# Optimization experiments

Hardware: AMD Instinct MI355X
Metric: run time of the kernel (lower is better)

Reference implementation:

```python
import jax, jax.numpy as jnp
import numpy as np

B, P, K_NN, HEADS = 4, 2048, 30, 3
N = B * P


def knn_nbr(feat):
    """Per-cloud exact KNN (no self), returns [N, K_NN+1] global neighbor idx, self appended last.
    Matches torch_geometric knn_graph (loop=False) followed by GATConv add_self_loops=True."""
    f = feat.reshape(B, P, -1)
    sq = jnp.sum(f * f, axis=-1)  # [B,P]
    d = sq[:, :, None] + sq[:, None, :] - 2.0 * jnp.einsum('bpc,bqc->bpq', f, f)
    d = d + jnp.eye(P, dtype=f.dtype)[None] * 1e9  # exclude self
    idx = jax.lax.top_k(-d, K_NN)[1]  # [B,P,K_NN] nearest neighbors
    idx = (idx + (jnp.arange(B) * P)[:, None, None]).reshape(N, K_NN)
    return jnp.concatenate([idx, jnp.arange(N)[:, None]], axis=1)  # self-loop last


def gat(xf, nbr, W, a_src, a_dst, bias):
    """PyG GATConv (v1, concat=True, negative_slope=0.2). nbr: [N,K] incoming sources per node."""
    H, F = a_src.shape
    xh = (xf @ W).reshape(N, H, F)
    s = jnp.sum(xh * a_src, axis=-1)  # [N,H] source scores
    t = jnp.sum(xh * a_dst, axis=-1)  # [N,H] target scores
    e = jax.nn.leaky_relu(s[nbr] + t[:, None, :], 0.2)  # [N,K,H]
    alpha = jax.nn.softmax(e, axis=1)  # edge-softmax over incoming edges
    out = jnp.einsum('nkh,nkhf->nhf', alpha, xh[nbr])
    return out.reshape(N, H * F) + bias


def setup_inputs() -> dict:
    key = jax.random.key(0)
    ks = jax.random.split(key, 48)
    w = lambda k, shape: (jax.random.normal(k, shape, jnp.float32) * 0.1)
    H = HEADS
    inp = {
        'x': jax.random.normal(ks[0], (N, 3), jnp.float32),
        'pos': jax.random.normal(ks[1], (N, 3), jnp.float32),
        'batch': (jnp.arange(N) // P).astype(jnp.int32),
        'w1': w(ks[2], (6, 64 * H)), 'as1': w(ks[3], (H, 64)), 'ad1': w(ks[4], (H, 64)), 'b1': w(ks[5], (64 * H,)),
        'ml1w': w(ks[6], (64 * H, 64)), 'ml1b': w(ks[7], (64,)),
        'w2': w(ks[8], (70, 64 * H)), 'as2': w(ks[9], (H, 64)), 'ad2': w(ks[10], (H, 64)), 'b2': w(ks[11], (64 * H,)),
        'ml2w': w(ks[12], (64 * H, 64)), 'ml2b': w(ks[13], (64,)),
        'w3': w(ks[14], (134, 64 * H)), 'as3': w(ks[15], (H, 64)), 'ad3': w(ks[16], (H, 64)), 'b3': w(ks[17], (64 * H,)),
        'ml3w': w(ks[18], (64 * H, 64)), 'ml3b': w(ks[19], (64,)),
        'w4': w(ks[20], (198, 128 * H)), 'as4': w(ks[21], (H, 128)), 'ad4': w(ks[22], (H, 128)), 'b4': w(ks[23], (128 * H,)),
        'ml4w': w(ks[24], (128 * H, 128)), 'ml4b': w(ks[25], (128,)),
        # fe_mlp: 326 -> 1024 -> 1024 (plain last)
        'few1': w(ks[26], (326, 1024)), 'feb1': w(ks[27], (1024,)),
        'few2': w(ks[28], (1024, 1024)), 'feb2': w(ks[29], (1024,)),
        # head mlp: 1350 -> 256 -> 256 -> 128 -> 50
        'mw1': w(ks[30], (1350, 256)), 'mb1': w(ks[31], (256,)),
        'mw2': w(ks[32], (256, 256)), 'mb2': w(ks[33], (256,)),
        'mw3': w(ks[34], (256, 128)), 'mb3': w(ks[35], (128,)),
        'mw4': w(ks[36], (128, 50)), 'mb4': w(ks[37], (50,)),
    }
    return inp


def reference(x, pos, batch,
              w1, as1, ad1, b1, ml1w, ml1b,
              w2, as2, ad2, b2, ml2w, ml2b,
              w3, as3, ad3, b3, ml3w, ml3b,
              w4, as4, ad4, b4, ml4w, ml4b,
              few1, feb1, few2, feb2,
              mw1, mb1, mw2, mb2, mw3, mb3, mw4, mb4):
    x0 = jnp.concatenate([x, pos], axis=-1)  # [N,6]
    nbr = knn_nbr(x0)
    x1 = gat(x0, nbr, w1, as1, ad1, b1) @ ml1w + ml1b  # [N,64]
    nbr = knn_nbr(x1)
    x2 = gat(jnp.concatenate([x0, x1], 1), nbr, w2, as2, ad2, b2) @ ml2w + ml2b
    nbr = knn_nbr(x2)
    x3 = gat(jnp.concatenate([x0, x1, x2], 1), nbr, w3, as3, ad3, b3) @ ml3w + ml3b
    nbr = knn_nbr(x2)  # faithful to source: 4th graph also built from x2
    x4 = gat(jnp.concatenate([x0, x1, x2, x3], 1), nbr, w4, as4, ad4, b4) @ ml4w + ml4b
    link4 = jnp.concatenate([x0, x1, x2, x3, x4], axis=-1)  # [N,326]
    h = jax.nn.relu(link4 @ few1 + feb1) @ few2 + feb2  # [N,1024]
    g = jnp.max(h, axis=0, keepdims=True)  # global feature (dropout=eval identity)
    lg = jnp.concatenate([link4, jnp.broadcast_to(g, (N, h.shape[1]))], axis=1)
    h = jax.nn.relu(lg @ mw1 + mb1)
    h = jax.nn.relu(h @ mw2 + mb2)
    h = jax.nn.relu(h @ mw3 + mb3)
    out = h @ mw4 + mb4
    return jax.nn.log_softmax(out, axis=1)
```

## Files before the change

kernel.cpp:

```cpp
#include <hip/hip_runtime.h>
#include <hip/hip_bf16.h>
#include <hip/amd_detail/amd_hip_vector_types.h>

#define NPTS 8192
#define PP 2048
#define KNN 30
#define KTOT 31
#define HEADS 3
#define LDH 352
#define NSEG 9
#define LDZ 200
#define LDZB3 200
#define LDZB4 392

typedef __attribute__((ext_vector_type(8))) short short8;
typedef __attribute__((ext_vector_type(4))) float floatx4;
typedef __attribute__((ext_vector_type(4))) unsigned int uint4_t;
typedef unsigned short ushort_t;
typedef unsigned int uint_t;

__device__ inline ushort_t f2bs(float v) {
    __hip_bfloat16 b = __float2bfloat16(v);
    return *reinterpret_cast<ushort_t*>(&b);
}
__device__ inline float bs2f(ushort_t u) {
    __hip_bfloat16 b = *reinterpret_cast<__hip_bfloat16*>(&u);
    return __bfloat162float(b);
}
__device__ inline void split2(float v, ushort_t& h, ushort_t& l) {
    h = f2bs(v);
    l = f2bs(v - bs2f(h));
}
__device__ inline uint_t fenc(float f) {
    uint_t b = __float_as_uint(f);
    return (b & 0x80000000u) ? ~b : (b | 0x80000000u);
}
__device__ inline float fdec(uint_t e) {
    return __uint_as_float((e & 0x80000000u) ? (e & 0x7FFFFFFFu) : ~e);
}

__global__ void k_build_x0(const float* __restrict__ x, const float* __restrict__ pos,
                           ushort_t* __restrict__ lh, ushort_t* __restrict__ ll) {
    int i = blockIdx.x * blockDim.x + threadIdx.x;
    if (i >= NPTS * 6) return;
    int n = i / 6, c = i % 6;
    float v = (c < 3) ? x[n * 3 + c] : pos[n * 3 + (c - 3)];
    ushort_t h, l; split2(v, h, l);
    lh[(size_t)n * LDH + c] = h;
    ll[(size_t)n * LDH + c] = l;
}

template<int F_>
__device__ inline void combine_body(const float* __restrict__ w, const float* __restrict__ mlw,
                                    const float* __restrict__ as_, const float* __restrict__ ad,
                                    const float* __restrict__ b, const float* __restrict__ mlb,
                                    float* __restrict__ wc, float* __restrict__ bc,
                                    int K_, int lb) {
    constexpr int NC = 3 * F_ + 6;
    constexpr int JG = 128 / F_;
    constexpr int RG = 8 / JG;
    int h = lb % 3, kb = lb / 3;
    int k0 = kb * 8, KS = min(8, K_ - k0);
    int tid = threadIdx.x;
    int j = tid % F_, rg = tid / F_;
    __shared__ float ws[8][F_];
    __shared__ float ms[32][F_];
    __shared__ float bav[3][F_];
    for (int idx = tid; idx < 8 * F_; idx += 128) {
        int r = idx / F_, f = idx % F_;
        ws[r][f] = (r < KS) ? w[(size_t)(k0 + r) * (3 * F_) + h * F_ + f] : 0.f;
    }
    for (int f = tid; f < F_; f += 128) {
        bav[0][f] = b[h * F_ + f];
        bav[1][f] = as_[h * F_ + f];
        bav[2][f] = ad[h * F_ + f];
    }
    __syncthreads();
    const float* mh = mlw + (size_t)h * F_ * F_;
    float acc[RG] = {};
    float bacc = 0.f;
    for (int f0 = 0; f0 < F_; f0 += 32) {
        for (int idx = tid; idx < 32 * F_; idx += 128) {
            int u = idx / F_, jj = idx % F_;
            ms[u][jj] = mh[(size_t)(f0 + u) * F_ + jj];
        }
        __syncthreads();
#pragma unroll
        for (int u = 0; u < 32; u++) {
            float m = ms[u][j];
#pragma unroll
            for (int r = 0; r < RG; r++)
                acc[r] += ws[rg * RG + r][f0 + u] * m;
            if (rg == 0) bacc += bav[0][f0 + u] * m;
        }
        __syncthreads();
    }
#pragma unroll
    for (int r = 0; r < RG; r++) {
        int k = k0 + rg * RG + r;
        if (k < K_) wc[(size_t)k * NC + h * F_ + j] = acc[r];
    }
    if (kb == 0 && rg == 0)
        atomicAdd(&bc[j], bacc + (h == 0 ? mlb[j] : 0.f));
    if (tid < 16) {
        int r = tid >> 1, sc = tid & 1;
        if (r < KS) {
            float s = 0.f;
#pragma unroll
            for (int f = 0; f < F_; f++) s += ws[r][f] * bav[1 + sc][f];
            wc[(size_t)(k0 + r) * NC + 3 * F_ + sc * 3 + h] = s;
        }
    }
}

struct C64 {
    const float *w[3], *mlw[3], *as_[3], *ad[3], *b[3], *mlb[3];
    float *wc[3], *bc[3];
    int K[3], t0[3];
};
__global__ __launch_bounds__(128)
void k_combine64(C64 a) {
    int bt = blockIdx.x, si = 0;
#pragma unroll
    for (int i = 1; i < 3; i++) if (bt >= a.t0[i]) si = i;
    combine_body<64>(a.w[si], a.mlw[si], a.as_[si], a.ad[si], a.b[si], a.mlb[si],
                     a.wc[si], a.bc[si], a.K[si], bt - a.t0[si]);
}
__global__ __launch_bounds__(128)
void k_combine128(const float* w, const float* mlw, const float* as_, const float* ad,
                  const float* b, const float* mlb, float* wc, float* bc, int K_) {
    combine_body<128>(w, mlw, as_, ad, b, mlb, wc, bc, K_, blockIdx.x);
}

__global__ void k_tw1(const float* __restrict__ x, const float* __restrict__ pos,
                      const float* __restrict__ wc, float* __restrict__ z) {
    int t = blockIdx.x * blockDim.x + threadIdx.x;
    if (t >= NPTS * 198) return;
    int n = t / 198, j = t % 198;
    float acc = 0.f;
#pragma unroll
    for (int c = 0; c < 3; c++) {
        acc += x[n * 3 + c] * wc[c * 198 + j];
        acc += pos[n * 3 + c] * wc[(3 + c) * 198 + j];
    }
    z[(size_t)n * LDZ + j] = acc;
}

struct WArgs {
    const float* src[NSEG];
    ushort_t* dst[NSEG];
    int K[NSEG], N[NSEG], Kp[NSEG], t0[NSEG];
};
__global__ void k_wsplit_all(WArgs a) {
    int bt = blockIdx.x;
    int si = 0;
#pragma unroll
    for (int i = 1; i < NSEG; i++) if (bt >= a.t0[i]) si = i;
    int t = bt - a.t0[si];
    int K_ = a.K[si], N_ = a.N[si], Kp = a.Kp[si];
    const float* src = a.src[si];
    ushort_t* dh = a.dst[si];
    ushort_t* dl = dh + (size_t)Kp * N_;
    int tX = (N_ + 31) >> 5;
    int k0 = (t / tX) * 32, n0 = (t % tX) * 32;
    __shared__ float tt[32][33];
    int c = threadIdx.x & 31, r8 = threadIdx.x >> 5;
#pragma unroll
    for (int i = 0; i < 4; i++) {
        int r = r8 + i * 8;
        int k = k0 + r, n = n0 + c;
        tt[r][c] = (k < K_ && n < N_) ? src[(size_t)k * N_ + n] : 0.f;
    }
    __syncthreads();
#pragma unroll
    for (int i = 0; i < 4; i++) {
        int r = r8 + i * 8;
        int n = n0 + r, k = k0 + c;
        if (n < N_) {
            float v = tt[c][r];
            ushort_t h, l; split2(v, h, l);
            dh[(size_t)n * Kp + k] = h;
            dl[(size_t)n * Kp + k] = l;
        }
    }
}

template<int MT, int NT>
__global__ __launch_bounds__(256)
void k_mgemm1(const ushort_t* __restrict__ A, int lda,
              const ushort_t* __restrict__ W, int ldw,
              float* __restrict__ Cf, int ldc,
              ushort_t* __restrict__ Ch, int ldh,
              int Ndim, int K,
              const float* __restrict__ bias1, const float* __restrict__ bias2,
              int relu, int lsm, uint_t* __restrict__ gmax) {
    constexpr int MTW = MT / 64;
    constexpr int NTT = NT / 16;
    __shared__ ushort_t As[2][MT * 40];
    __shared__ ushort_t Bs[2][NT * 40];
    __shared__ uint_t smax[NT];
    int tid = threadIdx.x;
    int w = tid >> 6, lane = tid & 63;
    int quad = lane >> 4, l16 = lane & 15;
    int m0 = blockIdx.x * MT, n0 = blockIdx.y * NT;
    uint4_t pa[MT / 64], pb[NT / 64];
    auto prefetch = [&](int k0) {
#pragma unroll
        for (int rep = 0; rep < MT / 64; rep++) {
            int idx = tid + rep * 256;
            int row = idx >> 2, q = idx & 3;
            pa[rep] = *(const uint4_t*)(A + (size_t)(m0 + row) * lda + k0 + q * 8);
        }
#pragma unroll
        for (int rep = 0; rep < NT / 64; rep++) {
            int idx = tid + rep * 256;
            int row = idx >> 2, q = idx & 3;
            uint4_t v = {0, 0, 0, 0};
            if (n0 + row < Ndim) v = *(const uint4_t*)(W + (size_t)(n0 + row) * ldw + k0 + q * 8);
            pb[rep] = v;
        }
    };
    auto stage = [&](int buf) {
#pragma unroll
        for (int rep = 0; rep < MT / 64; rep++) {
            int idx = tid + rep * 256;
            int row = idx >> 2, q = idx & 3;
            *(uint4_t*)&As[buf][row * 40 + q * 8] = pa[rep];
        }
#pragma unroll
        for (int rep = 0; rep < NT / 64; rep++) {
            int idx = tid + rep * 256;
            int row = idx >> 2, q = idx & 3;
            *(uint4_t*)&Bs[buf][row * 40 + q * 8] = pb[rep];
        }
    };
    if (gmax) {
        for (int idx = tid; idx < NT; idx += 256) smax[idx] = 0u;
    }
    floatx4 acc[MTW][NTT] = {};
    prefetch(0);
    stage(0);
    __syncthreads();
    int cur = 0;
    for (int k0 = 0; k0 < K; k0 += 32) {
        bool more = (k0 + 32 < K);
        if (more) prefetch(k0 + 32);
        short8 ah[MTW];
#pragma unroll
        for (int mt = 0; mt < MTW; mt++) {
            int r = w * (MT / 4) + mt * 16 + l16;
            ah[mt] = *(short8*)&As[cur][r * 40 + quad * 8];
        }
#pragma unroll
        for (int nt = 0; nt < NTT; nt++) {
            int r = nt * 16 + l16;
            short8 bh = *(short8*)&Bs[cur][r * 40 + quad * 8];
#pragma unroll
            for (int mt = 0; mt < MTW; mt++)
                acc[mt][nt] = __builtin_amdgcn_mfma_f32_16x16x32_bf16(ah[mt], bh, acc[mt][nt], 0, 0, 0);
        }
        if (more) stage(cur ^ 1);
        __syncthreads();
        cur ^= 1;
    }
    if (lsm) {
#pragma unroll
        for (int mt = 0; mt < MTW; mt++) {
#pragma unroll
            for (int r = 0; r < 4; r++) {
                float vv[NTT];
                float mrow = -3e38f;
#pragma unroll
                for (int nt = 0; nt < NTT; nt++) {
                    int n = n0 + nt * 16 + l16;
                    float val = (n < Ndim) ? acc[mt][nt][r] + bias1[n] : -3e38f;
                    vv[nt] = val;
                    mrow = fmaxf(mrow, val);
                }
#pragma unroll
                for (int off = 8; off >= 1; off >>= 1)
                    mrow = fmaxf(mrow, __shfl_xor(mrow, off, 64));
                float s = 0.f;
#pragma unroll
                for (int nt = 0; nt < NTT; nt++)
                    if (vv[nt] > -1e38f) s += expf(vv[nt] - mrow);
#pragma unroll
                for (int off = 8; off >= 1; off >>= 1)
                    s += __shfl_xor(s, off, 64);
                float lse = mrow + logf(s);
                int m = m0 + w * (MT / 4) + mt * 16 + quad * 4 + r;
#pragma unroll
                for (int nt = 0; nt < NTT; nt++) {
                    int n = n0 + nt * 16 + l16;
                    if (n < Ndim) Cf[(size_t)m * ldc + n] = vv[nt] - lse;
                }
            }
        }
        return;
    }
    if (gmax) {
#pragma unroll
        for (int mt = 0; mt < MTW; mt++) {
#pragma unroll
            for (int nt = 0; nt < NTT; nt++) {
#pragma unroll
                for (int r = 0; r < 4; r++) {
                    float v = acc[mt][nt][r] + bias1[nt * 16 + l16 + n0];
                    atomicMax(&smax[nt * 16 + l16], fenc(v));
                }
            }
        }
        __syncthreads();
        for (int idx = tid; idx < NT; idx += 256)
            atomicMax(&gmax[n0 + idx], smax[idx]);
        return;
    }
#pragma unroll
    for (int mt = 0; mt < MTW; mt++) {
#pragma unroll
        for (int nt = 0; nt < NTT; nt++) {
#pragma unroll
            for (int r = 0; r < 4; r++) {
                int m = m0 + w * (MT / 4) + mt * 16 + quad * 4 + r;
                int n = n0 + nt * 16 + l16;
                if (n < Ndim) {
                    float v = acc[mt][nt][r];
                    if (bias1) v += bias1[n];
                    if (bias2) v += bias2[n];
                    if (relu && v < 0.f) v = 0.f;
                    if (Cf) Cf[(size_t)m * ldc + n] = v;
                    if (Ch) Ch[(size_t)m * ldh + n] = f2bs(v);
                }
            }
        }
    }
}

__global__ __launch_bounds__(256)
void k_mgemm3(const ushort_t* __restrict__ Ah, const ushort_t* __restrict__ Al, int lda,
              const ushort_t* __restrict__ Wh, const ushort_t* __restrict__ Wl, int ldw,
              float* __restrict__ Cf, int ldc,
              int Ndim, int K) {
    constexpr int NTT = 4;
    __shared__ ushort_t AsH[64 * 40], BsH[64 * 40], AsL[64 * 40], BsL[64 * 40];
    int tid = threadIdx.x;
    int w = tid >> 6, lane = tid & 63;
    int quad = lane >> 4, l16 = lane & 15;
    int m0 = blockIdx.y * 64, n0 = blockIdx.x * 64;
    floatx4 acc[NTT] = {};
    for (int k0 = 0; k0 < K; k0 += 32) {
        {
            int row = tid >> 2, q = tid & 3;
            size_t go = (size_t)(m0 + row) * lda + k0 + q * 8;
            *(uint4_t*)&AsH[row * 40 + q * 8] = *(const uint4_t*)(Ah + go);
            *(uint4_t*)&AsL[row * 40 + q * 8] = *(const uint4_t*)(Al + go);
            uint4_t vh = {0, 0, 0, 0}, vl = {0, 0, 0, 0};
            size_t gw = (size_t)(n0 + row) * ldw + k0 + q * 8;
            if (n0 + row < Ndim) { vh = *(const uint4_t*)(Wh + gw); vl = *(const uint4_t*)(Wl + gw); }
            *(uint4_t*)&BsH[row * 40 + q * 8] = vh;
            *(uint4_t*)&BsL[row * 40 + q * 8] = vl;
        }
        __syncthreads();
        short8 ah, al;
        {
            int r = w * 16 + l16;
            ah = *(short8*)&AsH[r * 40 + quad * 8];
            al = *(short8*)&AsL[r * 40 + quad * 8];
        }
#pragma unroll
        for (int nt = 0; nt < NTT; nt++) {
            int r = nt * 16 + l16;
            short8 bh = *(short8*)&BsH[r * 40 + quad * 8];
            short8 bl = *(short8*)&BsL[r * 40 + quad * 8];
            acc[nt] = __builtin_amdgcn_mfma_f32_16x16x32_bf16(ah, bh, acc[nt], 0, 0, 0);
            acc[nt] = __builtin_amdgcn_mfma_f32_16x16x32_bf16(ah, bl, acc[nt], 0, 0, 0);
            acc[nt] = __builtin_amdgcn_mfma_f32_16x16x32_bf16(al, bh, acc[nt], 0, 0, 0);
        }
        __syncthreads();
    }
#pragma unroll
    for (int nt = 0; nt < NTT; nt++) {
#pragma unroll
        for (int r = 0; r < 4; r++) {
            int m = m0 + w * 16 + quad * 4 + r;
            int n = n0 + nt * 16 + l16;
            if (n < Ndim) Cf[(size_t)m * ldc + n] = acc[nt][r];
        }
    }
}

__global__ __launch_bounds__(256)
void k_mdist(const ushort_t* __restrict__ Lh, const ushort_t* __restrict__ Ll,
             int co, int C, uint_t* __restrict__ keys) {
    __shared__ ushort_t AsH[128 * 40], AsL[128 * 40], BsH[64 * 40], BsL[64 * 40];
    __shared__ float sqa[128], sqb[64];
    int tid = threadIdx.x;
    int w = tid >> 6, lane = tid & 63;
    int quad = lane >> 4, l16 = lane & 15;
    int b = blockIdx.z, cb = b * PP;
    int i0 = blockIdx.y * 128, j0 = blockIdx.x * 64;
    floatx4 acc[2][4] = {};
    float sacc = 0.f;
    for (int k0 = 0; k0 < C; k0 += 32) {
#pragma unroll
        for (int rep = 0; rep < 8; rep++) {
            int d = tid + rep * 256;
            int row = d >> 4, c2 = d & 15;
            size_t gi = ((size_t)(cb + i0 + row) * LDH + co + k0 + c2 * 2) >> 1;
            *(uint_t*)&AsH[row * 40 + c2 * 2] = ((const uint_t*)Lh)[gi];
            *(uint_t*)&AsL[row * 40 + c2 * 2] = ((const uint_t*)Ll)[gi];
        }
#pragma unroll
        for (int rep = 0; rep < 4; rep++) {
            int d = tid + rep * 256;
            int row = d >> 4, c2 = d & 15;
            size_t gi = ((size_t)(cb + j0 + row) * LDH + co + k0 + c2 * 2) >> 1;
            *(uint_t*)&BsH[row * 40 + c2 * 2] = ((const uint_t*)Lh)[gi];
            *(uint_t*)&BsL[row * 40 + c2 * 2] = ((const uint_t*)Ll)[gi];
        }
        __syncthreads();
        if (tid < 128) {
#pragma unroll
            for (int kk = 0; kk < 16; kk++) {
                uint_t ph = *(uint_t*)&AsH[tid * 40 + kk * 2];
                uint_t pl = *(uint_t*)&AsL[tid * 40 + kk * 2];
                float v0 = bs2f((ushort_t)(ph & 0xFFFFu)) + bs2f((ushort_t)(pl & 0xFFFFu));
                sacc += v0 * v0;
                float v1 = bs2f((ushort_t)(ph >> 16)) + bs2f((ushort_t)(pl >> 16));
                sacc += v1 * v1;
            }
        } else if (tid < 192) {
            int row = tid - 128;
#pragma unroll
            for (int kk = 0; kk < 16; kk++) {
                uint_t ph = *(uint_t*)&BsH[row * 40 + kk * 2];
                uint_t pl = *(uint_t*)&BsL[row * 40 + kk * 2];
                float v0 = bs2f((ushort_t)(ph & 0xFFFFu)) + bs2f((ushort_t)(pl & 0xFFFFu));
                sacc += v0 * v0;
                float v1 = bs2f((ushort_t)(ph >> 16)) + bs2f((ushort_t)(pl >> 16));
                sacc += v1 * v1;
            }
        }
        short8 ah[2], al[2];
#pragma unroll
        for (int mt = 0; mt < 2; mt++) {
            int r = w * 32 + mt * 16 + l16;
            ah[mt] = *(short8*)&AsH[r * 40 + quad * 8];
            al[mt] = *(short8*)&AsL[r * 40 + quad * 8];
        }
#pragma unroll
        for (int nt = 0; nt < 4; nt++) {
            int r = nt * 16 + l16;
            short8 bh = *(short8*)&BsH[r * 40 + quad * 8];
            short8 bl = *(short8*)&BsL[r * 40 + quad * 8];
#pragma unroll
            for (int mt = 0; mt < 2; mt++) {
                acc[mt][nt] = __builtin_amdgcn_mfma_f32_16x16x32_bf16(ah[mt], bh, acc[mt][nt], 0, 0, 0);
                acc[mt][nt] = __builtin_amdgcn_mfma_f32_16x16x32_bf16(ah[mt], bl, acc[mt][nt], 0, 0, 0);
                acc[mt][nt] = __builtin_amdgcn_mfma_f32_16x16x32_bf16(al[mt], bh, acc[mt][nt], 0, 0, 0);
            }
        }
        __syncthreads();
    }
    if (tid < 128) sqa[tid] = sacc;
    else if (tid < 192) sqb[tid - 128] = sacc;
    __syncthreads();
#pragma unroll
    for (int mt = 0; mt < 2; mt++) {
#pragma unroll
        for (int nt = 0; nt < 4; nt++) {
#pragma unroll
            for (int r = 0; r < 4; r++) {
                int li = w * 32 + mt * 16 + quad * 4 + r;
                int lj = nt * 16 + l16;
                int il = i0 + li, jl = j0 + lj;
                float dd = sqa[li] + sqb[lj] - 2.f * acc[mt][nt][r];
                dd = (il == jl) ? 3e9f : fmaxf(dd, 0.f);
                uint_t key = (__float_as_uint(dd) & 0xFFFFF800u) | (uint_t)jl;
                keys[(size_t)(cb + il) * PP + jl] = key;
            }
        }
    }
}

__global__ __launch_bounds__(256)
void k_topk(const uint_t* __restrict__ keys, int* __restrict__ nbr) {
    int r = blockIdx.x * 4 + (threadIdx.x >> 6);
    int lane = threadIdx.x & 63;
    int base = (r / PP) * PP;
    const uint_t* row = keys + (size_t)r * PP;
    uint_t v[32];
#pragma unroll
    for (int j = 0; j < 8; j++)
        *(uint4_t*)&v[j * 4] = *(const uint4_t*)(row + lane * 4 + j * 256);
    uint_t g[8];
#pragma unroll
    for (int j = 0; j < 8; j++)
        g[j] = min(min(v[j * 4], v[j * 4 + 1]), min(v[j * 4 + 2], v[j * 4 + 3]));
    uint_t lv = g[0];
#pragma unroll
    for (int j = 1; j < 8; j++) lv = min(lv, g[j]);
    for (int sel = 0; sel < KNN; sel++) {
        uint_t bk = lv;
#pragma unroll
        for (int off = 32; off > 0; off >>= 1)
            bk = min(bk, (uint_t)__shfl_xor((int)bk, off, 64));
        uint_t bks = __builtin_amdgcn_readfirstlane(bk);
        if (lane == 0) nbr[r * KTOT + sel] = base + (int)(bks & 0x7FFu);
        int grp = (int)((bks & 0x7FFu) >> 8);
#pragma unroll
        for (int jj = 0; jj < 8; jj++)
            if (grp == jj) {
#pragma unroll
                for (int t = 0; t < 4; t++)
                    v[jj * 4 + t] = (v[jj * 4 + t] == bks) ? 0xFFFFFFFFu : v[jj * 4 + t];
                g[jj] = min(min(v[jj * 4], v[jj * 4 + 1]), min(v[jj * 4 + 2], v[jj * 4 + 3]));
            }
        lv = g[0];
#pragma unroll
        for (int j = 1; j < 8; j++) lv = min(lv, g[j]);
    }
    if (lane == 0) nbr[r * KTOT + KNN] = r;
}

template<int F, int NN>
__global__ __launch_bounds__(192)
void k_gat2(const float* __restrict__ z, int ldz,
            const int* __restrict__ nbr,
            const float* __restrict__ bc,
            ushort_t* __restrict__ dh, ushort_t* __restrict__ dl) {
    constexpr int TPN = 3 * F / 4;
    __shared__ int srcs[NN][KTOT];
    __shared__ float alpha[NN][96];
    __shared__ float part[NN][2][F];
    int tid = threadIdx.x;
    if (tid < NN * KTOT) {
        int u = tid / KTOT, k = tid % KTOT;
        int t = blockIdx.x * NN + u;
        int node = (t & 3) * PP + (t >> 2);
        srcs[u][k] = nbr[node * KTOT + k];
    }
    __syncthreads();
#pragma unroll
    for (int u2 = 0; u2 < NN; u2 += 2) {
        int u = u2 + tid / 96;
        int r = tid % 96, h = r >> 5, k = r & 31;
        int t = blockIdx.x * NN + u;
        int node = (t & 3) * PP + (t >> 2);
        float e = -3e38f;
        if (k < KTOT) {
            float sv = z[(size_t)srcs[u][k] * ldz + 3 * F + h];
            float tv = z[(size_t)node * ldz + 3 * F + 3 + h];
            e = sv + tv;
            if (e < 0.f) e *= 0.2f;
        }
        float m = e;
#pragma unroll
        for (int off = 16; off >= 1; off >>= 1)
            m = fmaxf(m, __shfl_xor(m, off, 32));
        float ex = (k < KTOT) ? expf(e - m) : 0.f;
        float s = ex;
#pragma unroll
        for (int off = 16; off >= 1; off >>= 1)
            s += __shfl_xor(s, off, 32);
        alpha[u][h * 32 + k] = ex / s;
    }
    __syncthreads();
    {
        int u = tid / TPN, r = tid % TPN;
        int h = r / (F / 4), jq = r % (F / 4);
        const float* zb = z + h * F + jq * 4;
        floatx4 a0 = {0.f, 0.f, 0.f, 0.f}, a1 = {0.f, 0.f, 0.f, 0.f};
#pragma unroll
        for (int k = 0; k < KTOT; k += 2) {
            float a = alpha[u][h * 32 + k];
            floatx4 p = *(const floatx4*)(zb + (size_t)srcs[u][k] * ldz);
            a0 += p * a;
            if (k + 1 < KTOT) {
                float a2 = alpha[u][h * 32 + k + 1];
                floatx4 p2 = *(const floatx4*)(zb + (size_t)srcs[u][k + 1] * ldz);
                a1 += p2 * a2;
            }
        }
        floatx4 av = a0 + a1;
        if (h > 0)
            *(floatx4*)&part[u][h - 1][jq * 4] = av;
        __syncthreads();
        if (h == 0) {
            int t = blockIdx.x * NN + u;
            int node = (t & 3) * PP + (t >> 2);
            int j0 = jq * 4;
            floatx4 p0 = *(const floatx4*)&part[u][0][j0];
            floatx4 p1 = *(const floatx4*)&part[u][1][j0];
            floatx4 bcv = *(const floatx4*)&bc[j0];
            floatx4 v = av + p0 + p1 + bcv;
            ushort_t hh[4], ll[4];
#pragma unroll
            for (int q = 0; q < 4; q++) split2(v[q], hh[q], ll[q]);
            *(uint_t*)&dh[(size_t)node * LDH + j0] = (uint_t)hh[0] | ((uint_t)hh[1] << 16);
            *(uint_t*)&dh[(size_t)node * LDH + j0 + 2] = (uint_t)hh[2] | ((uint_t)hh[3] << 16);
            if (dl) {
                *(uint_t*)&dl[(size_t)node * LDH + j0] = (uint_t)ll[0] | ((uint_t)ll[1] << 16);
                *(uint_t*)&dl[(size_t)node * LDH + j0 + 2] = (uint_t)ll[2] | ((uint_t)ll[3] << 16);
            }
        }
    }
}

template<int F, int NN>
__global__ __launch_bounds__(192)
void k_gat2b(const ushort_t* __restrict__ z, int ldz,
             const int* __restrict__ nbr,
             const float* __restrict__ bc,
             ushort_t* __restrict__ dh) {
    constexpr int TPN = 3 * F / 8;
    __shared__ int srcs[NN][KTOT];
    __shared__ float alpha[NN][96];
    __shared__ float part[NN][2][F];
    int tid = threadIdx.x;
    for (int idx = tid; idx < NN * KTOT; idx += 192) {
        int u = idx / KTOT, k = idx % KTOT;
        int t = blockIdx.x * NN + u;
        int node = (t & 3) * PP + (t >> 2);
        srcs[u][k] = nbr[node * KTOT + k];
    }
    __syncthreads();
#pragma unroll
    for (int u2 = 0; u2 < NN; u2 += 2) {
        int u = u2 + tid / 96;
        int r = tid % 96, h = r >> 5, k = r & 31;
        int t = blockIdx.x * NN + u;
        int node = (t & 3) * PP + (t >> 2);
        float e = -3e38f;
        if (k < KTOT) {
            float sv = bs2f(z[(size_t)srcs[u][k] * ldz + 3 * F + h]);
            float tv = bs2f(z[(size_t)node * ldz + 3 * F + 3 + h]);
            e = sv + tv;
            if (e < 0.f) e *= 0.2f;
        }
        float m = e;
#pragma unroll
        for (int off = 16; off >= 1; off >>= 1)
            m = fmaxf(m, __shfl_xor(m, off, 32));
        float ex = (k < KTOT) ? expf(e - m) : 0.f;
        float s = ex;
#pragma unroll
        for (int off = 16; off >= 1; off >>= 1)
            s += __shfl_xor(s, off, 32);
        alpha[u][h * 32 + k] = ex / s;
    }
    __syncthreads();
    {
        int u = tid / TPN, r = tid % TPN;
        int h = r / (F / 8), jo = r % (F / 8);
        const ushort_t* zb = z + h * F + jo * 8;
        float a[8] = {};
        for (int k = 0; k < KTOT; k++) {
            float al = alpha[u][h * 32 + k];
            short8 v = *(const short8*)(zb + (size_t)srcs[u][k] * ldz);
#pragma unroll
            for (int q = 0; q < 8; q++)
                a[q] += al * bs2f((ushort_t)v[q]);
        }
        if (h > 0) {
#pragma unroll
            for (int q = 0; q < 8; q++) part[u][h - 1][jo * 8 + q] = a[q];
        }
        __syncthreads();
        if (h == 0) {
            int t = blockIdx.x * NN + u;
            int node = (t & 3) * PP + (t >> 2);
            int j0 = jo * 8;
#pragma unroll
            for (int q2 = 0; q2 < 4; q2++) {
                float v0 = a[q2 * 2] + part[u][0][j0 + q2 * 2] + part[u][1][j0 + q2 * 2] + bc[j0 + q2 * 2];
                float v1 = a[q2 * 2 + 1] + part[u][0][j0 + q2 * 2 + 1] + part[u][1][j0 + q2 * 2 + 1] + bc[j0 + q2 * 2 + 1];
                *(uint_t*)&dh[(size_t)node * LDH + j0 + q2 * 2] =
                    (uint_t)f2bs(v0) | ((uint_t)f2bs(v1) << 16);
            }
        }
    }
}

__global__ void k_gproj(const uint_t* __restrict__ genc,
                        const float* __restrict__ mw1,
                        const float* __restrict__ mb1,
                        float* __restrict__ gproj) {
    __shared__ float gs[128];
    int kb = blockIdx.x;
    int t = threadIdx.x;
    if (t < 128) gs[t] = fdec(genc[kb * 128 + t]);
    __syncthreads();
    float acc = (kb == 0) ? mb1[t] : 0.f;
    for (int k = 0; k < 128; k++)
        acc += gs[k] * mw1[(size_t)(326 + kb * 128 + k) * 256 + t];
    atomicAdd(&gproj[t], acc);
}

struct WT { ushort_t *h, *l; int kp; };

extern "C" void kernel_launch(void* const* d_in, const int* in_sizes, int n_in,
                              void* d_out, int out_size, void* d_ws, size_t ws_size,
                              hipStream_t stream) {
    (void)in_sizes; (void)n_in; (void)out_size; (void)ws_size;
    const float* x    = (const float*)d_in[0];
    const float* pos  = (const float*)d_in[1];
    const float* w1   = (const float*)d_in[3];
    const float* as1  = (const float*)d_in[4];
    const float* ad1  = (const float*)d_in[5];
    const float* b1   = (const float*)d_in[6];
    const float* ml1w = (const float*)d_in[7];
    const float* ml1b = (const float*)d_in[8];
    const float* w2   = (const float*)d_in[9];
    const float* as2  = (const float*)d_in[10];
    const float* ad2  = (const float*)d_in[11];
    const float* b2   = (const float*)d_in[12];
    const float* ml2w = (const float*)d_in[13];
    const float* ml2b = (const float*)d_in[14];
    const float* w3   = (const float*)d_in[15];
    const float* as3  = (const float*)d_in[16];
    const float* ad3  = (const float*)d_in[17];
    const float* b3   = (const float*)d_in[18];
    const float* ml3w = (const float*)d_in[19];
    const float* ml3b = (const float*)d_in[20];
    const float* w4   = (const float*)d_in[21];
    const float* as4  = (const float*)d_in[22];
    const float* ad4  = (const float*)d_in[23];
    const float* b4   = (const float*)d_in[24];
    const float* ml4w = (const float*)d_in[25];
    const float* ml4b = (const float*)d_in[26];
    const float* few1 = (const float*)d_in[27];
    const float* feb1 = (const float*)d_in[28];
    const float* few2 = (const float*)d_in[29];
    const float* feb2 = (const float*)d_in[30];
    const float* mw1  = (const float*)d_in[31];
    const float* mb1  = (const float*)d_in[32];
    const float* mw2  = (const float*)d_in[33];
    const float* mb2  = (const float*)d_in[34];
    const float* mw3  = (const float*)d_in[35];
    const float* mb3  = (const float*)d_in[36];
    const float* mw4  = (const float*)d_in[37];
    const float* mb4  = (const float*)d_in[38];

    float* Wb = (float*)d_ws;
    size_t off = 0;
    auto alloc = [&](size_t n) { float* p = Wb + off; off += (n + 63) & ~(size_t)63; return p; };

    float*    dist = alloc((size_t)NPTS * PP);
    ushort_t* l4h  = (ushort_t*)alloc((size_t)NPTS * LDH / 2);
    ushort_t* l4l  = (ushort_t*)alloc((size_t)NPTS * LDH / 2);
    uint_t* genc = (uint_t*)alloc(1024);
    float* gproj = alloc(256);
    float* bcp = alloc(320);
    float* bc1 = bcp, *bc2 = bcp + 64, *bc3 = bcp + 128, *bc4 = bcp + 192;
    int*   nbr   = (int*)alloc((size_t)NPTS * KTOT);
    ushort_t* wtpool = (ushort_t*)alloc(1742336);
    float* wc1 = alloc(6 * 198);
    float* wc2 = alloc(70 * 198);
    float* wc3 = alloc(134 * 198);
    float* wc4 = alloc(198 * 390);

    char* d0 = (char*)dist;
    uint_t*   dkey = (uint_t*)dist;
    float*    z    = dist;
    ushort_t* zb   = (ushort_t*)dist;
    ushort_t* hah  = (ushort_t*)d0;
    ushort_t* bBh  = (ushort_t*)(d0 + (size_t)NPTS * 1024 * 2);
    ushort_t* bAh = (ushort_t*)d0;
    ushort_t* bCh = (ushort_t*)d0;

    hipMemsetAsync(l4h, 0, (size_t)NPTS * LDH * 4, stream);
    hipMemsetAsync(genc, 0, (1024 + 256 + 320) * 4, stream);

    {
        C64 ca;
        const float* ws_[3] = {w1, w2, w3};
        const float* mlws[3] = {ml1w, ml2w, ml3w};
        const float* ass[3] = {as1, as2, as3};
        const float* ads[3] = {ad1, ad2, ad3};
        const float* bs_[3] = {b1, b2, b3};
        const float* mlbs[3] = {ml1b, ml2b, ml3b};
        float* wcs[3] = {wc1, wc2, wc3};
        float* bcs[3] = {bc1, bc2, bc3};
        int Ks[3] = {6, 70, 134};
        int t = 0;
        for (int i = 0; i < 3; i++) {
            ca.w[i] = ws_[i]; ca.mlw[i] = mlws[i]; ca.as_[i] = ass[i]; ca.ad[i] = ads[i];
            ca.b[i] = bs_[i]; ca.mlb[i] = mlbs[i]; ca.wc[i] = wcs[i]; ca.bc[i] = bcs[i];
            ca.K[i] = Ks[i]; ca.t0[i] = t;
            t += ((Ks[i] + 7) / 8) * 3;
        }
        k_combine64<<<t, 128, 0, stream>>>(ca);
        k_combine128<<<25 * 3, 128, 0, stream>>>(w4, ml4w, as4, ad4, b4, ml4b, wc4, bc4, 198);
    }

    WArgs wa;
    WT wt[NSEG];
    {
        const float* srcs[NSEG] = {wc2, wc3, wc4, few1, few2, mw1, mw2, mw3, mw4};
        int Ks[NSEG] = {70, 134, 198, 326, 1024, 326, 256, 256, 128};
        int Ns[NSEG] = {198, 198, 390, 1024, 1024, 256, 256, 128, 50};
        size_t wo = 0; int tiles = 0;
        for (int i = 0; i < NSEG; i++) {
            int kp = (Ks[i] + 31) & ~31;
            wa.src[i] = srcs[i];
            wa.dst[i] = wtpool + wo;
            wa.K[i] = Ks[i]; wa.N[i] = Ns[i]; wa.Kp[i] = kp;
            wa.t0[i] = tiles;
            wt[i] = { wtpool + wo, wtpool + wo + (size_t)kp * Ns[i], kp };
            wo += (size_t)2 * kp * Ns[i];
            tiles += (kp / 32) * ((Ns[i] + 31) / 32);
        }
        k_wsplit_all<<<tiles, 256, 0, stream>>>(wa);
    }
    WT tw2 = wt[0], tw3 = wt[1], tw4 = wt[2], tfe1 = wt[3], tfe2 = wt[4],
       tmw1 = wt[5], tmw2 = wt[6], tmw3 = wt[7], tmw4 = wt[8];

    auto mg3 = [&](const ushort_t* Ah, const ushort_t* Al, int lda, WT t,
                   float* Cf, int ldc, int Nd, int K) {
        dim3 g((Nd + 63) / 64, NPTS / 64);
        k_mgemm3<<<g, 256, 0, stream>>>(Ah, Al, lda, t.h, t.l, t.kp, Cf, ldc, Nd, K);
    };
    auto mg1 = [&](int MT, int NT, const ushort_t* Ah, int lda, WT t,
                   float* Cf, int ldc, ushort_t* Ch, int ldhh,
                   int Nd, int K, const float* bb1, const float* bb2,
                   int relu, int lsm, uint_t* gmax) {
        dim3 g(NPTS / MT, (Nd + NT - 1) / NT);
        if (MT == 128 && NT == 128)
            k_mgemm1<128, 128><<<g, 256, 0, stream>>>(Ah, lda, t.h, t.kp, Cf, ldc, Ch, ldhh, Nd, K,
                bb1, bb2, relu, lsm, gmax);
        else if (MT == 128)
            k_mgemm1<128, 64><<<g, 256, 0, stream>>>(Ah, lda, t.h, t.kp, Cf, ldc, Ch, ldhh, Nd, K,
                bb1, bb2, relu, lsm, gmax);
        else
            k_mgemm1<64, 64><<<g, 256, 0, stream>>>(Ah, lda, t.h, t.kp, Cf, ldc, Ch, ldhh, Nd, K,
                bb1, bb2, relu, lsm, gmax);
    };

    dim3 dgrid(PP / 64, PP / 128, 4);
    k_build_x0<<<(NPTS * 6 + 255) / 256, 256, 0, stream>>>(x, pos, l4h, l4l);

    k_mdist<<<dgrid, 256, 0, stream>>>(l4h, l4l, 0, 6, dkey);
    k_topk<<<NPTS / 4, 256, 0, stream>>>(dkey, nbr);
    k_tw1<<<(NPTS * 198 + 255) / 256, 256, 0, stream>>>(x, pos, wc1, z);
    k_gat2<64, 4><<<NPTS / 4, 192, 0, stream>>>(z, LDZ, nbr, bc1, l4h + 6, l4l + 6);

    k_mdist<<<dgrid, 256, 0, stream>>>(l4h, l4l, 6, 64, dkey);
    k_topk<<<NPTS / 4, 256, 0, stream>>>(dkey, nbr);
    mg3(l4h, l4l, LDH, tw2, z, LDZ, 198, 70);
    k_gat2<64, 4><<<NPTS / 4, 192, 0, stream>>>(z, LDZ, nbr, bc2, l4h + 70, l4l + 70);

    k_mdist<<<dgrid, 256, 0, stream>>>(l4h, l4l, 70, 64, dkey);
    k_topk<<<NPTS / 4, 256, 0, stream>>>(dkey, nbr);
    mg1(128, 64, l4h, LDH, tw3, nullptr, 0, zb, LDZB3, 198, 134, nullptr, nullptr, 0, 0, nullptr);
    k_gat2b<64, 8><<<NPTS / 8, 192, 0, stream>>>(zb, LDZB3, nbr, bc3, l4h + 134);

    mg1(128, 64, l4h, LDH, tw4, nullptr, 0, zb, LDZB4, 390, 198, nullptr, nullptr, 0, 0, nullptr);
    k_gat2b<128, 4><<<NPTS / 4, 192, 0, stream>>>(zb, LDZB4, nbr, bc4, l4h + 198);

    mg1(128, 128, l4h, LDH, tfe1, nullptr, 0, hah, 1024, 1024, 326, feb1, nullptr, 1, 0, nullptr);
    mg1(128, 128, hah, 1024, tfe2, nullptr, 0, nullptr, 0, 1024, 1024, feb2, nullptr, 0, 0, genc);
    k_gproj<<<8, 256, 0, stream>>>(genc, mw1, mb1, gproj);

    mg1(128, 64, l4h, LDH, tmw1, nullptr, 0, bAh, 256, 256, 326, nullptr, gproj, 1, 0, nullptr);
    mg1(128, 64, bAh, 256, tmw2, nullptr, 0, bBh, 256, 256, 256, mb2, nullptr, 1, 0, nullptr);
    mg1(64, 64, bBh, 256, tmw3, nullptr, 0, bCh, 128, 128, 256, mb3, nullptr, 1, 0, nullptr);
    mg1(64, 64, bCh, 128, tmw4, (float*)d_out, 50, nullptr, 0, 50, 128, mb4, nullptr, 0, 1, nullptr);
}
```

Before: 521.7 us.

## Fuse first-layer KNN distance and top-k into one register-resident kernel

Replaces the first-layer distance-matrix kernel and the separate top-k kernel with a single kernel. Each wave computes 6-dim fp32 distances for one row from shared memory and packs truncated distance bits with the index into a key. It then runs 30 rounds of wave-level min selection over 32 keys held in registers. This removes the global distance-key buffer write and read for the first graph. In exchange it truncates the low distance mantissa bits, which can change tie ordering among near-equal distances.

```diff
diff --git a/kernel.cpp b/kernel.cpp
--- a/kernel.cpp
+++ b/kernel.cpp
@@ -48,6 +48,74 @@
     ushort_t h, l; split2(v, h, l);
     lh[(size_t)n * LDH + c] = h;
     ll[(size_t)n * LDH + c] = l;
+}
+
+__global__ __launch_bounds__(256)
+void k_knn6(const float* __restrict__ x, const float* __restrict__ pos,
+            int* __restrict__ nbr) {
+    __shared__ float cs[6][PP];
+    __shared__ float sq[PP];
+    int tid = threadIdx.x;
+    int r0 = blockIdx.x * 4;
+    int cb = (r0 / PP) * PP;
+    for (int j = tid; j < PP; j += 256) {
+        float a0 = x[(size_t)(cb + j) * 3 + 0];
+        float a1 = x[(size_t)(cb + j) * 3 + 1];
+        float a2 = x[(size_t)(cb + j) * 3 + 2];
+        float p0 = pos[(size_t)(cb + j) * 3 + 0];
+        float p1 = pos[(size_t)(cb + j) * 3 + 1];
+        float p2 = pos[(size_t)(cb + j) * 3 + 2];
+        cs[0][j] = a0; cs[1][j] = a1; cs[2][j] = a2;
+        cs[3][j] = p0; cs[4][j] = p1; cs[5][j] = p2;
+        sq[j] = a0 * a0 + a1 * a1 + a2 * a2 + p0 * p0 + p1 * p1 + p2 * p2;
+    }
+    __syncthreads();
+    int w = tid >> 6, lane = tid & 63;
+    int rl = (r0 - cb) + w;
+    float c0 = cs[0][rl], c1 = cs[1][rl], c2 = cs[2][rl],
+          c3 = cs[3][rl], c4 = cs[4][rl], c5 = cs[5][rl];
+    float sqr = sq[rl];
+    uint_t v[32];
+#pragma unroll
+    for (int j8 = 0; j8 < 8; j8++)
+#pragma unroll
+        for (int t = 0; t < 4; t++) {
+            int jl = j8 * 256 + t * 64 + lane;
+            float dot = c0 * cs[0][jl] + c1 * cs[1][jl] + c2 * cs[2][jl]
+                      + c3 * cs[3][jl] + c4 * cs[4][jl] + c5 * cs[5][jl];
+            float dd = sqr + sq[jl] - 2.f * dot;
+            dd = (jl == rl) ? 3e9f : fmaxf(dd, 0.f);
+            v[j8 * 4 + t] = (__float_as_uint(dd) & 0xFFFFF800u) | (uint_t)jl;
+        }
+    uint_t g[8];
+#pragma unroll
+    for (int j = 0; j < 8; j++)
+        g[j] = min(min(v[j * 4], v[j * 4 + 1]), min(v[j * 4 + 2], v[j * 4 + 3]));
+    uint_t lv = g[0];
+#pragma unroll
+    for (int j = 1; j < 8; j++) lv = min(lv, g[j]);
+    int r = cb + rl;
+    for (int sel = 0; sel < KNN; sel++) {
+        uint_t bk = lv;
+#pragma unroll
+        for (int off = 32; off > 0; off >>= 1)
+            bk = min(bk, (uint_t)__shfl_xor((int)bk, off, 64));
+        uint_t bks = __builtin_amdgcn_readfirstlane(bk);
+        if (lane == 0) nbr[r * KTOT + sel] = cb + (int)(bks & 0x7FFu);
+        int grp = (int)((bks & 0x7FFu) >> 8);
+#pragma unroll
+        for (int jj = 0; jj < 8; jj++)
+            if (grp == jj) {
+#pragma unroll
+                for (int t = 0; t < 4; t++)
+                    v[jj * 4 + t] = (v[jj * 4 + t] == bks) ? 0xFFFFFFFFu : v[jj * 4 + t];
+                g[jj] = min(min(v[jj * 4], v[jj * 4 + 1]), min(v[jj * 4 + 2], v[jj * 4 + 3]));
+            }
+        lv = g[0];
+#pragma unroll
+        for (int j = 1; j < 8; j++) lv = min(lv, g[j]);
+    }
+    if (lane == 0) nbr[r * KTOT + KNN] = r;
 }
 
 template<int F_>
@@ -840,8 +908,7 @@
     dim3 dgrid(PP / 64, PP / 128, 4);
     k_build_x0<<<(NPTS * 6 + 255) / 256, 256, 0, stream>>>(x, pos, l4h, l4l);
 
-    k_mdist<<<dgrid, 256, 0, stream>>>(l4h, l4l, 0, 6, dkey);
-    k_topk<<<NPTS / 4, 256, 0, stream>>>(dkey, nbr);
+    k_knn6<<<NPTS / 4, 256, 0, stream>>>(x, pos, nbr);
     k_tw1<<<(NPTS * 198 + 255) / 256, 256, 0, stream>>>(x, pos, wc1, z);
     k_gat2<64, 4><<<NPTS / 4, 192, 0, stream>>>(z, LDZ, nbr, bc1, l4h + 6, l4l + 6);
 
```

Result: slower. 550.1 us (+5.4%).

## Fuse final two MLP layers with log-softmax and merge combine kernels

Applied to the files above, without the earlier changes.

Adds a head kernel that computes the third MLP layer into shared memory and then runs the final 128->50 layer and the row log-softmax in the same block, so the intermediate activation never goes to global memory. It also merges the two weight-combine launches into one kernel and folds the two memsets into one contiguous clear. Together these remove a few kernel launches and one global round-trip. The fused head runs at most 128 blocks of 64 rows, which may leave the GPU underused, and it assumes the genc buffer sits directly after l4h in memory.

```diff
diff --git a/kernel.cpp b/kernel.cpp
--- a/kernel.cpp
+++ b/kernel.cpp
@@ -113,23 +113,24 @@
     }
 }
 
-struct C64 {
-    const float *w[3], *mlw[3], *as_[3], *ad[3], *b[3], *mlb[3];
-    float *wc[3], *bc[3];
-    int K[3], t0[3];
+struct CAll {
+    const float *w[4], *mlw[4], *as_[4], *ad[4], *b[4], *mlb[4];
+    float *wc[4], *bc[4];
+    int K[4], t0[4], t64;
 };
 __global__ __launch_bounds__(128)
-void k_combine64(C64 a) {
-    int bt = blockIdx.x, si = 0;
-#pragma unroll
-    for (int i = 1; i < 3; i++) if (bt >= a.t0[i]) si = i;
-    combine_body<64>(a.w[si], a.mlw[si], a.as_[si], a.ad[si], a.b[si], a.mlb[si],
-                     a.wc[si], a.bc[si], a.K[si], bt - a.t0[si]);
-}
-__global__ __launch_bounds__(128)
-void k_combine128(const float* w, const float* mlw, const float* as_, const float* ad,
-                  const float* b, const float* mlb, float* wc, float* bc, int K_) {
-    combine_body<128>(w, mlw, as_, ad, b, mlb, wc, bc, K_, blockIdx.x);
+void k_combine_all(CAll a) {
+    int bt = blockIdx.x;
+    if (bt < a.t64) {
+        int si = 0;
+#pragma unroll
+        for (int i = 1; i < 3; i++) if (bt >= a.t0[i]) si = i;
+        combine_body<64>(a.w[si], a.mlw[si], a.as_[si], a.ad[si], a.b[si], a.mlb[si],
+                         a.wc[si], a.bc[si], a.K[si], bt - a.t0[si]);
+    } else {
+        combine_body<128>(a.w[3], a.mlw[3], a.as_[3], a.ad[3], a.b[3], a.mlb[3],
+                          a.wc[3], a.bc[3], a.K[3], bt - a.t64);
+    }
 }
 
 __global__ void k_tw1(const float* __restrict__ x, const float* __restrict__ pos,
@@ -332,6 +333,102 @@
                     if (Ch) Ch[(size_t)m * ldh + n] = f2bs(v);
                 }
             }
+        }
+    }
+}
+
+__global__ __launch_bounds__(256)
+void k_head34(const ushort_t* __restrict__ A, int lda,
+              const ushort_t* __restrict__ W3, int ldw3,
+              const ushort_t* __restrict__ W4, int ldw4,
+              const float* __restrict__ mb3, const float* __restrict__ mb4,
+              float* __restrict__ out) {
+    __shared__ ushort_t As[64 * 40];
+    __shared__ ushort_t Bs[128 * 40];
+    __shared__ ushort_t C1[64 * 136];
+    int tid = threadIdx.x;
+    int w = tid >> 6, lane = tid & 63;
+    int quad = lane >> 4, l16 = lane & 15;
+    int m0 = blockIdx.x * 64;
+    floatx4 acc[8] = {};
+    for (int k0 = 0; k0 < 256; k0 += 32) {
+        {
+            int row = tid >> 2, q = tid & 3;
+            *(uint4_t*)&As[row * 40 + q * 8] =
+                *(const uint4_t*)(A + (size_t)(m0 + row) * lda + k0 + q * 8);
+#pragma unroll
+            for (int rep = 0; rep < 2; rep++) {
+                int idx = tid + rep * 256;
+                int br = idx >> 2, bq = idx & 3;
+                *(uint4_t*)&Bs[br * 40 + bq * 8] =
+                    *(const uint4_t*)(W3 + (size_t)br * ldw3 + k0 + bq * 8);
+            }
+        }
+        __syncthreads();
+        short8 ah = *(short8*)&As[(w * 16 + l16) * 40 + quad * 8];
+#pragma unroll
+        for (int nt = 0; nt < 8; nt++) {
+            short8 bh = *(short8*)&Bs[(nt * 16 + l16) * 40 + quad * 8];
+            acc[nt] = __builtin_amdgcn_mfma_f32_16x16x32_bf16(ah, bh, acc[nt], 0, 0, 0);
+        }
+        __syncthreads();
+    }
+#pragma unroll
+    for (int nt = 0; nt < 8; nt++) {
+#pragma unroll
+        for (int r = 0; r < 4; r++) {
+            int rowl = w * 16 + quad * 4 + r;
+            int col = nt * 16 + l16;
+            float v = acc[nt][r] + mb3[col];
+            if (v < 0.f) v = 0.f;
+            C1[rowl * 136 + col] = f2bs(v);
+        }
+    }
+    __syncthreads();
+    floatx4 acc2[4] = {};
+    for (int k0 = 0; k0 < 128; k0 += 32) {
+        {
+            int row = tid >> 2, q = tid & 3;
+            uint4_t v = {0, 0, 0, 0};
+            if (row < 50) v = *(const uint4_t*)(W4 + (size_t)row * ldw4 + k0 + q * 8);
+            *(uint4_t*)&Bs[row * 40 + q * 8] = v;
+        }
+        __syncthreads();
+        short8 ah = *(short8*)&C1[(w * 16 + l16) * 136 + k0 + quad * 8];
+#pragma unroll
+        for (int nt = 0; nt < 4; nt++) {
+            short8 bh = *(short8*)&Bs[(nt * 16 + l16) * 40 + quad * 8];
+            acc2[nt] = __builtin_amdgcn_mfma_f32_16x16x32_bf16(ah, bh, acc2[nt], 0, 0, 0);
+        }
+        __syncthreads();
+    }
+#pragma unroll
+    for (int r = 0; r < 4; r++) {
+        float vv[4];
+        float mrow = -3e38f;
+#pragma unroll
+        for (int nt = 0; nt < 4; nt++) {
+            int n = nt * 16 + l16;
+            float val = (n < 50) ? acc2[nt][r] + mb4[n] : -3e38f;
+            vv[nt] = val;
+            mrow = fmaxf(mrow, val);
+        }
+#pragma unroll
+        for (int off = 8; off >= 1; off >>= 1)
+            mrow = fmaxf(mrow, __shfl_xor(mrow, off, 64));
+        float s = 0.f;
+#pragma unroll
+        for (int nt = 0; nt < 4; nt++)
+            if (vv[nt] > -1e38f) s += expf(vv[nt] - mrow);
+#pragma unroll
+        for (int off = 8; off >= 1; off >>= 1)
+            s += __shfl_xor(s, off, 64);
+        float lse = mrow + logf(s);
+        int m = m0 + w * 16 + quad * 4 + r;
+#pragma unroll
+        for (int nt = 0; nt < 4; nt++) {
+            int n = nt * 16 + l16;
+            if (n < 50) out[(size_t)m * 50 + n] = vv[nt] - lse;
         }
     }
 }
@@ -767,31 +864,30 @@
     ushort_t* hah  = (ushort_t*)d0;
     ushort_t* bBh  = (ushort_t*)(d0 + (size_t)NPTS * 1024 * 2);
     ushort_t* bAh = (ushort_t*)d0;
-    ushort_t* bCh = (ushort_t*)d0;
-
-    hipMemsetAsync(l4h, 0, (size_t)NPTS * LDH * 4, stream);
-    hipMemsetAsync(genc, 0, (1024 + 256 + 320) * 4, stream);
+
+    hipMemsetAsync(l4h, 0, ((size_t)NPTS * LDH + 1600) * 4, stream);
 
     {
-        C64 ca;
-        const float* ws_[3] = {w1, w2, w3};
-        const float* mlws[3] = {ml1w, ml2w, ml3w};
-        const float* ass[3] = {as1, as2, as3};
-        const float* ads[3] = {ad1, ad2, ad3};
-        const float* bs_[3] = {b1, b2, b3};
-        const float* mlbs[3] = {ml1b, ml2b, ml3b};
-        float* wcs[3] = {wc1, wc2, wc3};
-        float* bcs[3] = {bc1, bc2, bc3};
-        int Ks[3] = {6, 70, 134};
+        CAll ca;
+        const float* ws_[4] = {w1, w2, w3, w4};
+        const float* mlws[4] = {ml1w, ml2w, ml3w, ml4w};
+        const float* ass[4] = {as1, as2, as3, as4};
+        const float* ads[4] = {ad1, ad2, ad3, ad4};
+        const float* bs_[4] = {b1, b2, b3, b4};
+        const float* mlbs[4] = {ml1b, ml2b, ml3b, ml4b};
+        float* wcs[4] = {wc1, wc2, wc3, wc4};
+        float* bcs[4] = {bc1, bc2, bc3, bc4};
+        int Ks[4] = {6, 70, 134, 198};
         int t = 0;
-        for (int i = 0; i < 3; i++) {
+        for (int i = 0; i < 4; i++) {
             ca.w[i] = ws_[i]; ca.mlw[i] = mlws[i]; ca.as_[i] = ass[i]; ca.ad[i] = ads[i];
             ca.b[i] = bs_[i]; ca.mlb[i] = mlbs[i]; ca.wc[i] = wcs[i]; ca.bc[i] = bcs[i];
-            ca.K[i] = Ks[i]; ca.t0[i] = t;
-            t += ((Ks[i] + 7) / 8) * 3;
-        }
-        k_combine64<<<t, 128, 0, stream>>>(ca);
-        k_combine128<<<25 * 3, 128, 0, stream>>>(w4, ml4w, as4, ad4, b4, ml4b, wc4, bc4, 198);
+            ca.K[i] = Ks[i];
+            if (i < 3) { ca.t0[i] = t; t += ((Ks[i] + 7) / 8) * 3; }
+        }
+        ca.t64 = t;
+        int total = t + 25 * 3;
+        k_combine_all<<<total, 128, 0, stream>>>(ca);
     }
 
     WArgs wa;
@@ -864,6 +960,6 @@
 
     mg1(128, 64, l4h, LDH, tmw1, nullptr, 0, bAh, 256, 256, 326, nullptr, gproj, 1, 0, nullptr);
     mg1(128, 64, bAh, 256, tmw2, nullptr, 0, bBh, 256, 256, 256, mb2, nullptr, 1, 0, nullptr);
-    mg1(64, 64, bBh, 256, tmw3, nullptr, 0, bCh, 128, 128, 256, mb3, nullptr, 1, 0, nullptr);
-    mg1(64, 64, bCh, 128, tmw4, (float*)d_out, 50, nullptr, 0, 50, 128, mb4, nullptr, 0, 1, nullptr);
-}
+    k_head34<<<NPTS / 64, 256, 0, stream>>>(bBh, 256, tmw3.h, tmw3.kp, tmw4.h, tmw4.kp,
+                                            mb3, mb4, (float*)d_out);
+}
```

New measurement: 503.9 us. -3.4%, faster.
